# Optimization experiments

Hardware: AMD Instinct MI355X
Metric: run time of the kernel (lower is better)

The kernel has to match this reference:

```python
import jax, jax.numpy as jnp
import numpy as np

B, N, D = 4096, 64, 128
H, ATT = 8, 32
SCALE = ATT ** -0.5


def setup_inputs() -> dict:
    key = jax.random.key(0)
    k1, k2, k3, k4, k5 = jax.random.split(key, 5)
    x = jax.random.normal(k1, (B, N, D), dtype=jnp.float32)
    # glorot-ish scale for weights
    W_Q = jax.random.normal(k2, (H, D, ATT), dtype=jnp.float32) * (2.0 / (D + ATT)) ** 0.5
    W_K = jax.random.normal(k3, (H, D, ATT), dtype=jnp.float32) * (2.0 / (D + ATT)) ** 0.5
    W_V = jax.random.normal(k4, (H, D, ATT), dtype=jnp.float32) * (2.0 / (D + ATT)) ** 0.5
    W_res = jax.random.normal(k5, (D, H * ATT), dtype=jnp.float32) * (2.0 / (D + H * ATT)) ** 0.5
    return {"x": x, "W_Q": W_Q, "W_K": W_K, "W_V": W_V, "W_res": W_res}


def reference(x, W_Q, W_K, W_V, W_res):
    # per-head projections: (B,N,D) x (H,D,K) -> (B,H,N,K)
    Q = jnp.einsum('bnd,hdk->bhnk', x, W_Q)
    K = jnp.einsum('bnd,hdk->bhnk', x, W_K)
    V = jnp.einsum('bnd,hdk->bhnk', x, W_V)
    scores = jnp.einsum('bhnk,bhmk->bhnm', Q, K) * SCALE  # (B,H,N,N)
    attn = jax.nn.softmax(scores, axis=-1)
    ctx = jnp.einsum('bhnm,bhmk->bhnk', attn, V)          # (B,H,N,K)
    ctx = ctx.transpose(0, 2, 1, 3).reshape(x.shape[0], x.shape[1], H * ATT)
    res = x @ W_res  # d != H*att_dim -> residual projection
    return jax.nn.relu(ctx + res)
```

## Files before the change

### kernel.cpp

```cpp
#include <hip/hip_runtime.h>

#define NB    4096
#define SEQ   64
#define DIM   128
#define NHEAD 8
#define ATTD  32
#define HKC   256
#define SCALE 0.17677669529663687f
#define LOG2E 1.4426950408889634f

typedef __bf16 bf16_t;
typedef __bf16 bf16x8 __attribute__((ext_vector_type(8)));
typedef __bf16 bf16x4 __attribute__((ext_vector_type(4)));
typedef float  f32x4  __attribute__((ext_vector_type(4)));
typedef unsigned int u32;

static __device__ __forceinline__ bf16_t f2bf(float f) {
  unsigned u = __builtin_bit_cast(unsigned, f);
  u = (u + 0x7FFFu + ((u >> 16) & 1u)) >> 16;
  unsigned short s = (unsigned short)u;
  return __builtin_bit_cast(bf16_t, s);
}

static __device__ __forceinline__ u32 pkbf(float a, float b) {
  unsigned ua = __builtin_bit_cast(unsigned, a);
  ua = (ua + 0x7FFFu + ((ua >> 16) & 1u)) >> 16;
  unsigned ub = __builtin_bit_cast(unsigned, b);
  ub = (ub + 0x7FFFu + ((ub >> 16) & 1u)) & 0xFFFF0000u;
  return (ua & 0xFFFFu) | ub;
}

static __device__ __forceinline__ bf16x8 merge2(f32x4 t0, f32x4 t1, int lo, int g) {
  u32 p0 = pkbf(t0[0], t0[1]);
  u32 p1 = pkbf(t0[2], t0[3]);
  u32 q0 = pkbf(t1[0], t1[1]);
  u32 q1 = pkbf(t1[2], t1[3]);
  const int srcA = lo + ((g & 1) << 5);
  const int srcB = srcA + 16;
  u32 a0 = (u32)__shfl((int)p0, srcA, 64);
  u32 a1 = (u32)__shfl((int)p1, srcA, 64);
  u32 b0 = (u32)__shfl((int)p0, srcB, 64);
  u32 b1 = (u32)__shfl((int)p1, srcB, 64);
  u32 c0 = (u32)__shfl((int)q0, srcA, 64);
  u32 c1 = (u32)__shfl((int)q1, srcA, 64);
  u32 d0 = (u32)__shfl((int)q0, srcB, 64);
  u32 d1 = (u32)__shfl((int)q1, srcB, 64);
  const bool glow = (g < 2);
  union { u32 u[4]; bf16x8 v; } r;
  r.u[0] = glow ? a0 : c0;
  r.u[1] = glow ? a1 : c1;
  r.u[2] = glow ? b0 : d0;
  r.u[3] = glow ? b1 : d1;
  return r.v;
}

#define XSWZ(r, c) (((r) << 7) + ((c) ^ (((r) & 7) << 3)))
#define VSWZ(r, c) (((r) << 6) + ((c) ^ (((r) & 7) << 3)))
#define PSWZ(r, c) (((r) << 6) + ((c) ^ (((r) & 7) << 3)))

__global__ void prep_weights(const float* __restrict__ Wq,
                             const float* __restrict__ Wk,
                             const float* __restrict__ Wv,
                             const float* __restrict__ Wr,
                             bf16_t* __restrict__ ws) {
  int idx = blockIdx.x * 256 + threadIdx.x;
  int m = idx >> 15;
  int e = idx & 32767;
  int c = e >> 7;
  int d = e & 127;
  float v;
  if (m == 0)      v = Wq[((c >> 5) * DIM + d) * ATTD + (c & 31)] * (SCALE * LOG2E);
  else if (m == 1) v = Wk[((c >> 5) * DIM + d) * ATTD + (c & 31)];
  else if (m == 2) v = Wv[((c >> 5) * DIM + d) * ATTD + (c & 31)];
  else             v = Wr[d * HKC + c];
  ws[idx] = f2bf(v);
}

__launch_bounds__(256, 3)
__global__ void fused_attn(const float* __restrict__ xg,
                           const bf16_t* __restrict__ ws,
                           float* __restrict__ outg) {
  __shared__ bf16_t Xb[64 * 128];
  __shared__ bf16_t Vt[4][32 * 64];
  __shared__ bf16_t Pt[4][16 * 64];

  const int t  = threadIdx.x;
  const int w  = t >> 6;
  const int l  = t & 63;
  const int lo = l & 15;
  const int g  = l >> 4;
  const int b  = blockIdx.x;

  {
    const float* xb = xg + (size_t)b * (SEQ * DIM);
#pragma unroll
    for (int i = 0; i < 8; ++i) {
      int idx = i * 1024 + t * 4;
      float4 v = *(const float4*)(xb + idx);
      bf16x4 p;
      p[0] = f2bf(v.x); p[1] = f2bf(v.y); p[2] = f2bf(v.z); p[3] = f2bf(v.w);
      *(bf16x4*)&Xb[XSWZ(idx >> 7, idx & 127)] = p;
    }
  }
  __syncthreads();

  const bf16_t* wsq = ws;
  const bf16_t* wsk = ws + 32768;
  const bf16_t* wsv = ws + 65536;
  const bf16_t* wsr = ws + 98304;
  float* ob = outg + (size_t)b * (SEQ * HKC);
  const f32x4 z4 = {0.f, 0.f, 0.f, 0.f};

#pragma unroll
  for (int hh = 0; hh < 2; ++hh) {
    const int hc = w * 64 + hh * 32;

    f32x4 acck[2][4];
#pragma unroll
    for (int i = 0; i < 2; ++i)
#pragma unroll
      for (int j = 0; j < 4; ++j) acck[i][j] = z4;
#pragma unroll
    for (int kk = 0; kk < 4; ++kk) {
      bf16x8 aw[2], bx[4];
#pragma unroll
      for (int at = 0; at < 2; ++at)
        aw[at] = *(const bf16x8*)(wsk + (hc + at * 16 + lo) * DIM + kk * 32 + g * 8);
#pragma unroll
      for (int nt = 0; nt < 4; ++nt)
        bx[nt] = *(const bf16x8*)&Xb[XSWZ(nt * 16 + lo, kk * 32 + g * 8)];
#pragma unroll
      for (int at = 0; at < 2; ++at)
#pragma unroll
        for (int nt = 0; nt < 4; ++nt)
          acck[at][nt] = __builtin_amdgcn_mfma_f32_16x16x32_bf16(aw[at], bx[nt], acck[at][nt], 0, 0, 0);
    }
    bf16x8 kf[4];
#pragma unroll
    for (int nt = 0; nt < 4; ++nt) kf[nt] = merge2(acck[0][nt], acck[1][nt], lo, g);

    f32x4 accv[4][2];
#pragma unroll
    for (int i = 0; i < 4; ++i)
#pragma unroll
      for (int j = 0; j < 2; ++j) accv[i][j] = z4;
#pragma unroll
    for (int kk = 0; kk < 4; ++kk) {
      bf16x8 ax[4], bw[2];
#pragma unroll
      for (int nt = 0; nt < 4; ++nt)
        ax[nt] = *(const bf16x8*)&Xb[XSWZ(nt * 16 + lo, kk * 32 + g * 8)];
#pragma unroll
      for (int ct = 0; ct < 2; ++ct)
        bw[ct] = *(const bf16x8*)(wsv + (hc + ct * 16 + lo) * DIM + kk * 32 + g * 8);
#pragma unroll
      for (int nt = 0; nt < 4; ++nt)
#pragma unroll
        for (int ct = 0; ct < 2; ++ct)
          accv[nt][ct] = __builtin_amdgcn_mfma_f32_16x16x32_bf16(ax[nt], bw[ct], accv[nt][ct], 0, 0, 0);
    }
#pragma unroll
    for (int nt = 0; nt < 4; ++nt)
#pragma unroll
      for (int ct = 0; ct < 2; ++ct) {
        uint2 d;
        d.x = pkbf(accv[nt][ct][0], accv[nt][ct][1]);
        d.y = pkbf(accv[nt][ct][2], accv[nt][ct][3]);
        *(uint2*)&Vt[w][VSWZ(ct * 16 + lo, nt * 16 + 4 * g)] = d;
      }

    f32x4 accq[2][4];
#pragma unroll
    for (int i = 0; i < 2; ++i)
#pragma unroll
      for (int j = 0; j < 4; ++j) accq[i][j] = z4;
#pragma unroll
    for (int kk = 0; kk < 4; ++kk) {
      bf16x8 aw[2], bx[4];
#pragma unroll
      for (int at = 0; at < 2; ++at)
        aw[at] = *(const bf16x8*)(wsq + (hc + at * 16 + lo) * DIM + kk * 32 + g * 8);
#pragma unroll
      for (int mt = 0; mt < 4; ++mt)
        bx[mt] = *(const bf16x8*)&Xb[XSWZ(mt * 16 + lo, kk * 32 + g * 8)];
#pragma unroll
      for (int at = 0; at < 2; ++at)
#pragma unroll
        for (int mt = 0; mt < 4; ++mt)
          accq[at][mt] = __builtin_amdgcn_mfma_f32_16x16x32_bf16(aw[at], bx[mt], accq[at][mt], 0, 0, 0);
    }
    bf16x8 qf[4];
#pragma unroll
    for (int mt = 0; mt < 4; ++mt) qf[mt] = merge2(accq[0][mt], accq[1][mt], lo, g);

    bf16x8 vf[2][2];
#pragma unroll
    for (int ct = 0; ct < 2; ++ct)
#pragma unroll
      for (int kk2 = 0; kk2 < 2; ++kk2)
        vf[ct][kk2] = *(const bf16x8*)&Vt[w][VSWZ(ct * 16 + lo, kk2 * 32 + g * 8)];

    f32x4 ch[2][4];
#pragma unroll
    for (int mt = 0; mt < 4; ++mt) {
      f32x4 sv[4];
#pragma unroll
      for (int nt = 0; nt < 4; ++nt)
        sv[nt] = __builtin_amdgcn_mfma_f32_16x16x32_bf16(kf[nt], qf[mt], z4, 0, 0, 0);
      float sum = 0.f;
#pragma unroll
      for (int nt = 0; nt < 4; ++nt)
#pragma unroll
        for (int j = 0; j < 4; ++j) {
          float e = __builtin_amdgcn_exp2f(sv[nt][j]);
          sv[nt][j] = e;
          sum += e;
        }
#pragma unroll
      for (int nt = 0; nt < 4; ++nt) {
        uint2 d;
        d.x = pkbf(sv[nt][0], sv[nt][1]);
        d.y = pkbf(sv[nt][2], sv[nt][3]);
        *(uint2*)&Pt[w][PSWZ(lo, nt * 16 + 4 * g)] = d;
      }
      sum += __shfl_xor(sum, 16, 64);
      sum += __shfl_xor(sum, 32, 64);
      float rinv = __builtin_amdgcn_rcpf(sum);
      bf16x8 pf0 = *(const bf16x8*)&Pt[w][PSWZ(lo, g * 8)];
      bf16x8 pf1 = *(const bf16x8*)&Pt[w][PSWZ(lo, 32 + g * 8)];
#pragma unroll
      for (int ct = 0; ct < 2; ++ct) {
        f32x4 a = __builtin_amdgcn_mfma_f32_16x16x32_bf16(vf[ct][0], pf0, z4, 0, 0, 0);
        a = __builtin_amdgcn_mfma_f32_16x16x32_bf16(vf[ct][1], pf1, a, 0, 0, 0);
        ch[ct][mt] = a * rinv;
      }
    }

#pragma unroll
    for (int kk = 0; kk < 4; ++kk) {
      bf16x8 aw[2], bx[4];
#pragma unroll
      for (int ct = 0; ct < 2; ++ct)
        aw[ct] = *(const bf16x8*)(wsr + (hc + ct * 16 + lo) * DIM + kk * 32 + g * 8);
#pragma unroll
      for (int mt = 0; mt < 4; ++mt)
        bx[mt] = *(const bf16x8*)&Xb[XSWZ(mt * 16 + lo, kk * 32 + g * 8)];
#pragma unroll
      for (int ct = 0; ct < 2; ++ct)
#pragma unroll
        for (int mt = 0; mt < 4; ++mt)
          ch[ct][mt] = __builtin_amdgcn_mfma_f32_16x16x32_bf16(aw[ct], bx[mt], ch[ct][mt], 0, 0, 0);
    }

#pragma unroll
    for (int ct = 0; ct < 2; ++ct)
#pragma unroll
      for (int mt = 0; mt < 4; ++mt) {
        float4 o;
        o.x = fmaxf(ch[ct][mt][0], 0.f);
        o.y = fmaxf(ch[ct][mt][1], 0.f);
        o.z = fmaxf(ch[ct][mt][2], 0.f);
        o.w = fmaxf(ch[ct][mt][3], 0.f);
        *(float4*)(ob + (mt * 16 + lo) * HKC + hc + ct * 16 + 4 * g) = o;
      }
  }
}

extern "C" void kernel_launch(void* const* d_in, const int* in_sizes, int n_in,
                              void* d_out, int out_size, void* d_ws, size_t ws_size,
                              hipStream_t stream) {
  const float* x  = (const float*)d_in[0];
  const float* Wq = (const float*)d_in[1];
  const float* Wk = (const float*)d_in[2];
  const float* Wv = (const float*)d_in[3];
  const float* Wr = (const float*)d_in[4];
  bf16_t* ws = (bf16_t*)d_ws;
  float* out = (float*)d_out;

  prep_weights<<<512, 256, 0, stream>>>(Wq, Wk, Wv, Wr, ws);
  fused_attn<<<NB, 256, 0, stream>>>(x, ws, out);
}
```

Before: 203.8 us.

## Fuse K/V and Q/residual projection loops and reuse one per-wave LDS buffer

The K and V projections now share one k-loop, and so do the Q and residual projections, so each X fragment is read from LDS once per pair instead of twice. The shuffle-based merge2 transpose of the K and Q accumulators is replaced with a bf16 round trip through LDS. V, K, Q and P staging now share a single per-wave LDS buffer, which cuts shared memory per block. Manual bf16 rounding is replaced with native casts. The residual accumulators stay live through the softmax/attention phase, which raises register pressure under the 3-block launch bound and risks spills.

```diff
diff --git a/kernel.cpp b/kernel.cpp
--- a/kernel.cpp
+++ b/kernel.cpp
@@ -15,46 +15,14 @@
 typedef float  f32x4  __attribute__((ext_vector_type(4)));
 typedef unsigned int u32;
 
-static __device__ __forceinline__ bf16_t f2bf(float f) {
-  unsigned u = __builtin_bit_cast(unsigned, f);
-  u = (u + 0x7FFFu + ((u >> 16) & 1u)) >> 16;
-  unsigned short s = (unsigned short)u;
-  return __builtin_bit_cast(bf16_t, s);
-}
-
 static __device__ __forceinline__ u32 pkbf(float a, float b) {
-  unsigned ua = __builtin_bit_cast(unsigned, a);
-  ua = (ua + 0x7FFFu + ((ua >> 16) & 1u)) >> 16;
-  unsigned ub = __builtin_bit_cast(unsigned, b);
-  ub = (ub + 0x7FFFu + ((ub >> 16) & 1u)) & 0xFFFF0000u;
-  return (ua & 0xFFFFu) | ub;
-}
-
-static __device__ __forceinline__ bf16x8 merge2(f32x4 t0, f32x4 t1, int lo, int g) {
-  u32 p0 = pkbf(t0[0], t0[1]);
-  u32 p1 = pkbf(t0[2], t0[3]);
-  u32 q0 = pkbf(t1[0], t1[1]);
-  u32 q1 = pkbf(t1[2], t1[3]);
-  const int srcA = lo + ((g & 1) << 5);
-  const int srcB = srcA + 16;
-  u32 a0 = (u32)__shfl((int)p0, srcA, 64);
-  u32 a1 = (u32)__shfl((int)p1, srcA, 64);
-  u32 b0 = (u32)__shfl((int)p0, srcB, 64);
-  u32 b1 = (u32)__shfl((int)p1, srcB, 64);
-  u32 c0 = (u32)__shfl((int)q0, srcA, 64);
-  u32 c1 = (u32)__shfl((int)q1, srcA, 64);
-  u32 d0 = (u32)__shfl((int)q0, srcB, 64);
-  u32 d1 = (u32)__shfl((int)q1, srcB, 64);
-  const bool glow = (g < 2);
-  union { u32 u[4]; bf16x8 v; } r;
-  r.u[0] = glow ? a0 : c0;
-  r.u[1] = glow ? a1 : c1;
-  r.u[2] = glow ? b0 : d0;
-  r.u[3] = glow ? b1 : d1;
-  return r.v;
+  unsigned short ua = __builtin_bit_cast(unsigned short, (__bf16)a);
+  unsigned short ub = __builtin_bit_cast(unsigned short, (__bf16)b);
+  return (u32)ua | ((u32)ub << 16);
 }
 
 #define XSWZ(r, c) (((r) << 7) + ((c) ^ (((r) & 7) << 3)))
+#define WSWZ(r, c) (((r) << 5) + ((c) ^ (((r) & 3) << 3)))
 #define VSWZ(r, c) (((r) << 6) + ((c) ^ (((r) & 7) << 3)))
 #define PSWZ(r, c) (((r) << 6) + ((c) ^ (((r) & 7) << 3)))
 
@@ -73,7 +41,7 @@
   else if (m == 1) v = Wk[((c >> 5) * DIM + d) * ATTD + (c & 31)];
   else if (m == 2) v = Wv[((c >> 5) * DIM + d) * ATTD + (c & 31)];
   else             v = Wr[d * HKC + c];
-  ws[idx] = f2bf(v);
+  ws[idx] = (bf16_t)v;
 }
 
 __launch_bounds__(256, 3)
@@ -81,8 +49,7 @@
                            const bf16_t* __restrict__ ws,
                            float* __restrict__ outg) {
   __shared__ bf16_t Xb[64 * 128];
-  __shared__ bf16_t Vt[4][32 * 64];
-  __shared__ bf16_t Pt[4][16 * 64];
+  __shared__ bf16_t VP[4][2048];
 
   const int t  = threadIdx.x;
   const int w  = t >> 6;
@@ -91,6 +58,8 @@
   const int g  = l >> 4;
   const int b  = blockIdx.x;
 
+  bf16_t* const vp = VP[w];
+
   {
     const float* xb = xg + (size_t)b * (SEQ * DIM);
 #pragma unroll
@@ -98,7 +67,7 @@
       int idx = i * 1024 + t * 4;
       float4 v = *(const float4*)(xb + idx);
       bf16x4 p;
-      p[0] = f2bf(v.x); p[1] = f2bf(v.y); p[2] = f2bf(v.z); p[3] = f2bf(v.w);
+      p[0] = (bf16_t)v.x; p[1] = (bf16_t)v.y; p[2] = (bf16_t)v.z; p[3] = (bf16_t)v.w;
       *(bf16x4*)&Xb[XSWZ(idx >> 7, idx & 127)] = p;
     }
   }
@@ -116,49 +85,53 @@
     const int hc = w * 64 + hh * 32;
 
     f32x4 acck[2][4];
+    f32x4 accv[4][2];
 #pragma unroll
     for (int i = 0; i < 2; ++i)
 #pragma unroll
       for (int j = 0; j < 4; ++j) acck[i][j] = z4;
 #pragma unroll
+    for (int i = 0; i < 4; ++i)
+#pragma unroll
+      for (int j = 0; j < 2; ++j) accv[i][j] = z4;
+#pragma unroll
     for (int kk = 0; kk < 4; ++kk) {
-      bf16x8 aw[2], bx[4];
-#pragma unroll
-      for (int at = 0; at < 2; ++at)
-        aw[at] = *(const bf16x8*)(wsk + (hc + at * 16 + lo) * DIM + kk * 32 + g * 8);
+      bf16x8 bx[4], awk[2], bwv[2];
 #pragma unroll
       for (int nt = 0; nt < 4; ++nt)
         bx[nt] = *(const bf16x8*)&Xb[XSWZ(nt * 16 + lo, kk * 32 + g * 8)];
 #pragma unroll
       for (int at = 0; at < 2; ++at)
+        awk[at] = *(const bf16x8*)(wsk + (hc + at * 16 + lo) * DIM + kk * 32 + g * 8);
+#pragma unroll
+      for (int ct = 0; ct < 2; ++ct)
+        bwv[ct] = *(const bf16x8*)(wsv + (hc + ct * 16 + lo) * DIM + kk * 32 + g * 8);
+#pragma unroll
+      for (int at = 0; at < 2; ++at)
 #pragma unroll
         for (int nt = 0; nt < 4; ++nt)
-          acck[at][nt] = __builtin_amdgcn_mfma_f32_16x16x32_bf16(aw[at], bx[nt], acck[at][nt], 0, 0, 0);
-    }
+          acck[at][nt] = __builtin_amdgcn_mfma_f32_16x16x32_bf16(awk[at], bx[nt], acck[at][nt], 0, 0, 0);
+#pragma unroll
+      for (int nt = 0; nt < 4; ++nt)
+#pragma unroll
+        for (int ct = 0; ct < 2; ++ct)
+          accv[nt][ct] = __builtin_amdgcn_mfma_f32_16x16x32_bf16(bx[nt], bwv[ct], accv[nt][ct], 0, 0, 0);
+    }
+
+#pragma unroll
+    for (int at = 0; at < 2; ++at)
+#pragma unroll
+      for (int nt = 0; nt < 4; ++nt) {
+        uint2 d;
+        d.x = pkbf(acck[at][nt][0], acck[at][nt][1]);
+        d.y = pkbf(acck[at][nt][2], acck[at][nt][3]);
+        *(uint2*)&vp[WSWZ(nt * 16 + lo, at * 16 + 4 * g)] = d;
+      }
     bf16x8 kf[4];
 #pragma unroll
-    for (int nt = 0; nt < 4; ++nt) kf[nt] = merge2(acck[0][nt], acck[1][nt], lo, g);
-
-    f32x4 accv[4][2];
-#pragma unroll
-    for (int i = 0; i < 4; ++i)
-#pragma unroll
-      for (int j = 0; j < 2; ++j) accv[i][j] = z4;
-#pragma unroll
-    for (int kk = 0; kk < 4; ++kk) {
-      bf16x8 ax[4], bw[2];
-#pragma unroll
-      for (int nt = 0; nt < 4; ++nt)
-        ax[nt] = *(const bf16x8*)&Xb[XSWZ(nt * 16 + lo, kk * 32 + g * 8)];
-#pragma unroll
-      for (int ct = 0; ct < 2; ++ct)
-        bw[ct] = *(const bf16x8*)(wsv + (hc + ct * 16 + lo) * DIM + kk * 32 + g * 8);
-#pragma unroll
-      for (int nt = 0; nt < 4; ++nt)
-#pragma unroll
-        for (int ct = 0; ct < 2; ++ct)
-          accv[nt][ct] = __builtin_amdgcn_mfma_f32_16x16x32_bf16(ax[nt], bw[ct], accv[nt][ct], 0, 0, 0);
-    }
+    for (int nt = 0; nt < 4; ++nt)
+      kf[nt] = *(const bf16x8*)&vp[WSWZ(nt * 16 + lo, 8 * g)];
+
 #pragma unroll
     for (int nt = 0; nt < 4; ++nt)
 #pragma unroll
@@ -166,41 +139,59 @@
         uint2 d;
         d.x = pkbf(accv[nt][ct][0], accv[nt][ct][1]);
         d.y = pkbf(accv[nt][ct][2], accv[nt][ct][3]);
-        *(uint2*)&Vt[w][VSWZ(ct * 16 + lo, nt * 16 + 4 * g)] = d;
-      }
+        *(uint2*)&vp[VSWZ(ct * 16 + lo, nt * 16 + 4 * g)] = d;
+      }
+    bf16x8 vf[2][2];
+#pragma unroll
+    for (int ct = 0; ct < 2; ++ct)
+#pragma unroll
+      for (int kk2 = 0; kk2 < 2; ++kk2)
+        vf[ct][kk2] = *(const bf16x8*)&vp[VSWZ(ct * 16 + lo, kk2 * 32 + g * 8)];
 
     f32x4 accq[2][4];
+    f32x4 accr[2][4];
 #pragma unroll
     for (int i = 0; i < 2; ++i)
 #pragma unroll
-      for (int j = 0; j < 4; ++j) accq[i][j] = z4;
+      for (int j = 0; j < 4; ++j) { accq[i][j] = z4; accr[i][j] = z4; }
 #pragma unroll
     for (int kk = 0; kk < 4; ++kk) {
-      bf16x8 aw[2], bx[4];
-#pragma unroll
-      for (int at = 0; at < 2; ++at)
-        aw[at] = *(const bf16x8*)(wsq + (hc + at * 16 + lo) * DIM + kk * 32 + g * 8);
+      bf16x8 bx[4], awq[2], awr[2];
 #pragma unroll
       for (int mt = 0; mt < 4; ++mt)
         bx[mt] = *(const bf16x8*)&Xb[XSWZ(mt * 16 + lo, kk * 32 + g * 8)];
 #pragma unroll
       for (int at = 0; at < 2; ++at)
+        awq[at] = *(const bf16x8*)(wsq + (hc + at * 16 + lo) * DIM + kk * 32 + g * 8);
+#pragma unroll
+      for (int ct = 0; ct < 2; ++ct)
+        awr[ct] = *(const bf16x8*)(wsr + (hc + ct * 16 + lo) * DIM + kk * 32 + g * 8);
+#pragma unroll
+      for (int at = 0; at < 2; ++at)
 #pragma unroll
         for (int mt = 0; mt < 4; ++mt)
-          accq[at][mt] = __builtin_amdgcn_mfma_f32_16x16x32_bf16(aw[at], bx[mt], accq[at][mt], 0, 0, 0);
-    }
+          accq[at][mt] = __builtin_amdgcn_mfma_f32_16x16x32_bf16(awq[at], bx[mt], accq[at][mt], 0, 0, 0);
+#pragma unroll
+      for (int ct = 0; ct < 2; ++ct)
+#pragma unroll
+        for (int mt = 0; mt < 4; ++mt)
+          accr[ct][mt] = __builtin_amdgcn_mfma_f32_16x16x32_bf16(awr[ct], bx[mt], accr[ct][mt], 0, 0, 0);
+    }
+
+#pragma unroll
+    for (int at = 0; at < 2; ++at)
+#pragma unroll
+      for (int mt = 0; mt < 4; ++mt) {
+        uint2 d;
+        d.x = pkbf(accq[at][mt][0], accq[at][mt][1]);
+        d.y = pkbf(accq[at][mt][2], accq[at][mt][3]);
+        *(uint2*)&vp[WSWZ(mt * 16 + lo, at * 16 + 4 * g)] = d;
+      }
     bf16x8 qf[4];
 #pragma unroll
-    for (int mt = 0; mt < 4; ++mt) qf[mt] = merge2(accq[0][mt], accq[1][mt], lo, g);
-
-    bf16x8 vf[2][2];
-#pragma unroll
-    for (int ct = 0; ct < 2; ++ct)
-#pragma unroll
-      for (int kk2 = 0; kk2 < 2; ++kk2)
-        vf[ct][kk2] = *(const bf16x8*)&Vt[w][VSWZ(ct * 16 + lo, kk2 * 32 + g * 8)];
-
-    f32x4 ch[2][4];
+    for (int mt = 0; mt < 4; ++mt)
+      qf[mt] = *(const bf16x8*)&vp[WSWZ(mt * 16 + lo, 8 * g)];
+
 #pragma unroll
     for (int mt = 0; mt < 4; ++mt) {
       f32x4 sv[4];
@@ -221,35 +212,21 @@
         uint2 d;
         d.x = pkbf(sv[nt][0], sv[nt][1]);
         d.y = pkbf(sv[nt][2], sv[nt][3]);
-        *(uint2*)&Pt[w][PSWZ(lo, nt * 16 + 4 * g)] = d;
+        *(uint2*)&vp[PSWZ(lo, nt * 16 + 4 * g)] = d;
       }
       sum += __shfl_xor(sum, 16, 64);
       sum += __shfl_xor(sum, 32, 64);
       float rinv = __builtin_amdgcn_rcpf(sum);
-      bf16x8 pf0 = *(const bf16x8*)&Pt[w][PSWZ(lo, g * 8)];
-      bf16x8 pf1 = *(const bf16x8*)&Pt[w][PSWZ(lo, 32 + g * 8)];
+      bf16x8 pf0 = *(const bf16x8*)&vp[PSWZ(lo, g * 8)];
+      bf16x8 pf1 = *(const bf16x8*)&vp[PSWZ(lo, 32 + g * 8)];
 #pragma unroll
       for (int ct = 0; ct < 2; ++ct) {
         f32x4 a = __builtin_amdgcn_mfma_f32_16x16x32_bf16(vf[ct][0], pf0, z4, 0, 0, 0);
         a = __builtin_amdgcn_mfma_f32_16x16x32_bf16(vf[ct][1], pf1, a, 0, 0, 0);
-        ch[ct][mt] = a * rinv;
-      }
-    }
-
-#pragma unroll
-    for (int kk = 0; kk < 4; ++kk) {
-      bf16x8 aw[2], bx[4];
-#pragma unroll
-      for (int ct = 0; ct < 2; ++ct)
-        aw[ct] = *(const bf16x8*)(wsr + (hc + ct * 16 + lo) * DIM + kk * 32 + g * 8);
-#pragma unroll
-      for (int mt = 0; mt < 4; ++mt)
-        bx[mt] = *(const bf16x8*)&Xb[XSWZ(mt * 16 + lo, kk * 32 + g * 8)];
-#pragma unroll
-      for (int ct = 0; ct < 2; ++ct)
-#pragma unroll
-        for (int mt = 0; mt < 4; ++mt)
-          ch[ct][mt] = __builtin_amdgcn_mfma_f32_16x16x32_bf16(aw[ct], bx[mt], ch[ct][mt], 0, 0, 0);
+#pragma unroll
+        for (int j = 0; j < 4; ++j)
+          accr[ct][mt][j] = fmaf(a[j], rinv, accr[ct][mt][j]);
+      }
     }
 
 #pragma unroll
@@ -257,10 +234,10 @@
 #pragma unroll
       for (int mt = 0; mt < 4; ++mt) {
         float4 o;
-        o.x = fmaxf(ch[ct][mt][0], 0.f);
-        o.y = fmaxf(ch[ct][mt][1], 0.f);
-        o.z = fmaxf(ch[ct][mt][2], 0.f);
-        o.w = fmaxf(ch[ct][mt][3], 0.f);
+        o.x = fmaxf(accr[ct][mt][0], 0.f);
+        o.y = fmaxf(accr[ct][mt][1], 0.f);
+        o.z = fmaxf(accr[ct][mt][2], 0.f);
+        o.w = fmaxf(accr[ct][mt][3], 0.f);
         *(float4*)(ob + (mt * 16 + lo) * HKC + hc + ct * 16 + 4 * g) = o;
       }
   }
```

Measured after the change: 274.4 us. +34.7%, slower.
